# Kernel optimization log

Measured on AMD Instinct MI355X. Metric: run time of the kernel, lower is better.

## Reference

```python
import jax, jax.numpy as jnp
import numpy as np
from jax import lax

D = 1024
K = 3
LN_EPS = 1e-5


def setup_inputs() -> dict:
    key = jax.random.key(0)
    ks = jax.random.split(key, 8)
    B, T = 8, 4096
    x = jax.random.normal(ks[0], (B, T, D), dtype=jnp.float32)
    s = 1.0 / np.sqrt(D)
    in_proj_w = jax.random.uniform(ks[1], (D, 2 * D), jnp.float32, -s, s)
    in_proj_b = jax.random.uniform(ks[2], (2 * D,), jnp.float32, -s, s)
    conv_w = jax.random.uniform(ks[3], (D, 1, K), jnp.float32, -1.0 / np.sqrt(K), 1.0 / np.sqrt(K))
    conv_b = jax.random.uniform(ks[4], (D,), jnp.float32, -1.0 / np.sqrt(K), 1.0 / np.sqrt(K))
    logit_a = jnp.zeros((D,), jnp.float32)
    ssm_b = jnp.full((D,), 0.1, jnp.float32)
    ssm_c = jnp.ones((D,), jnp.float32)
    ssm_d = jnp.zeros((D,), jnp.float32)
    out_proj_w = jax.random.uniform(ks[5], (D, D), jnp.float32, -s, s)
    out_proj_b = jax.random.uniform(ks[6], (D,), jnp.float32, -s, s)
    ln_w = jnp.ones((D,), jnp.float32)
    ln_b = jnp.zeros((D,), jnp.float32)
    return {"x": x, "in_proj_w": in_proj_w, "in_proj_b": in_proj_b,
            "conv_w": conv_w, "conv_b": conv_b, "logit_a": logit_a,
            "ssm_b": ssm_b, "ssm_c": ssm_c, "ssm_d": ssm_d,
            "out_proj_w": out_proj_w, "out_proj_b": out_proj_b,
            "ln_w": ln_w, "ln_b": ln_b}


def _dwconv(v, conv_w, conv_b):
    # v: (B, T, D) -> depthwise conv1d, kernel K, 'same' padding
    vt = jnp.transpose(v, (0, 2, 1))  # (B, D, T)
    out = lax.conv_general_dilated(
        vt, conv_w, window_strides=(1,), padding=[(K // 2, K // 2)],
        dimension_numbers=("NCH", "OIH", "NCH"), feature_group_count=D)
    out = out + conv_b[None, :, None]
    return jnp.transpose(out, (0, 2, 1))  # (B, T, D)


def reference(x, in_proj_w, in_proj_b, conv_w, conv_b, logit_a,
              ssm_b, ssm_c, ssm_d, out_proj_w, out_proj_b, ln_w, ln_b):
    B, T, _ = x.shape
    residual = x
    uv = x @ in_proj_w + in_proj_b                      # (B, T, 2D)
    u, v = uv[..., :D], uv[..., D:]
    v = jax.nn.silu(v)
    v_local = _dwconv(v, conv_w, conv_b)                # (B, T, D)

    a = jax.nn.sigmoid(logit_a).astype(v_local.dtype)
    # diagonal LTI scan: h_t = a*h_{t-1} + b*u_t ; y_t = c*h_t + d*u_t
    def step(h, vt):
        h = a * h + ssm_b * vt
        return h, ssm_c * h + ssm_d * vt
    h0 = jnp.zeros((B, D), v_local.dtype)
    _, y_seq = lax.scan(step, h0, jnp.transpose(v_local, (1, 0, 2)))
    y_seq = jnp.transpose(y_seq, (1, 0, 2))             # (B, T, D)

    out = u * jax.nn.silu(y_seq)
    out = out @ out_proj_w + out_proj_b                 # dropout: eval mode (identity)
    h = out + residual
    mu = jnp.mean(h, axis=-1, keepdims=True)
    var = jnp.mean(jnp.square(h - mu), axis=-1, keepdims=True)
    return (h - mu) * lax.rsqrt(var + LN_EPS) * ln_w + ln_b
```

## Files before the change

### kernel.cpp

```cpp
#include <hip/hip_runtime.h>
#include <cstdint>
#include <cstddef>

#define D_DIM   1024
#define TWO_D   2048
#define B_DIM   8
#define T_DIM   4096
#define BT_DIM  (B_DIM*T_DIM)
#define LN_EPS  1e-5f
#define NCHUNK  128
#define CLEN    (T_DIM/NCHUNK)

typedef __attribute__((ext_vector_type(8))) short bf16x8;
typedef __attribute__((ext_vector_type(4))) float f32x4;

__device__ __forceinline__ float bf2f(unsigned short u){
  union { unsigned int i; float f; } c; c.i = ((unsigned int)u) << 16; return c.f;
}
__device__ __forceinline__ unsigned short f2bf(float f){
  union { float f; unsigned int i; } c; c.f = f;
  unsigned int x = c.i;
  return (unsigned short)((x + 0x7fffu + ((x >> 16) & 1u)) >> 16);
}
__device__ __forceinline__ float sigmoidf_(float x){ return 1.f/(1.f+__expf(-x)); }
__device__ __forceinline__ float siluf_(float x){ return x/(1.f+__expf(-x)); }


__global__ void cvt_f32_bf16(const float* __restrict__ in, unsigned short* __restrict__ out, int n){
  int i = (blockIdx.x*blockDim.x + threadIdx.x)*4;
  const int stride = gridDim.x*blockDim.x*4;
  for (; i + 3 < n; i += stride){
    float4 f = *(const float4*)(in + i);
    ushort4 o; o.x=f2bf(f.x); o.y=f2bf(f.y); o.z=f2bf(f.z); o.w=f2bf(f.w);
    *(ushort4*)(out + i) = o;
  }
}

__global__ __launch_bounds__(256) void cvt_transpose(
    const float* __restrict__ W, unsigned short* __restrict__ Wt,
    int rows, int cols)
{
  __shared__ float tile[32][33];
  const int tx = threadIdx.x & 31;
  const int ty = threadIdx.x >> 5;
  const int tpc = cols >> 5;
  const int bc = blockIdx.x % tpc;
  const int br = blockIdx.x / tpc;
  const int gc = bc*32 + tx;
  const int gr = br*32;
#pragma unroll
  for (int i = 0; i < 32; i += 8)
    tile[ty + i][tx] = W[(size_t)(gr + ty + i)*cols + gc];
  __syncthreads();
#pragma unroll
  for (int i = 0; i < 32; i += 8)
    Wt[(size_t)(bc*32 + ty + i)*rows + gr + tx] = f2bf(tile[tx][ty + i]);
}

template<int EPI>
__global__ __launch_bounds__(1024) void gemm256(
    const unsigned short* __restrict__ A,
    const unsigned short* __restrict__ Bt,
    const float* __restrict__ bias,
    const float* __restrict__ resid,
    unsigned short* __restrict__ outU,
    unsigned short* __restrict__ outV,
    const int K, const int nbn)
{
  __shared__ __align__(16) unsigned short sA[2][2][8192];
  __shared__ __align__(16) unsigned short sB[2][2][8192];

#define BARRIER()   __builtin_amdgcn_s_barrier()
#define FENCE()     __builtin_amdgcn_sched_barrier(0)
#define WAIT_VM2()  do { asm volatile("s_waitcnt vmcnt(2)"); FENCE(); } while(0)
#define WAIT_VM0()  do { asm volatile("s_waitcnt vmcnt(0)"); FENCE(); } while(0)

  const int tid  = threadIdx.x;
  const int lane = tid & 63;
  const int wv   = tid >> 6;
  const int wr   = wv >> 2;
  const int wc   = wv & 3;
  const int fr   = lane & 15;
  const int fq   = lane >> 4;

  const int nwg = gridDim.x;
  const int cpx = nwg >> 3;
  const int wg  = (blockIdx.x & 7) * cpx + (blockIdx.x >> 3);
  const int bm = wg / nbn, bn = wg % nbn;

  const unsigned short* Ag = A  + (size_t)bm * 256 * K;
  const unsigned short* Bg = Bt + (size_t)bn * 256 * K;

  const int r0  = tid >> 2;
  const int c0  = tid & 3;
  const int cs0 = c0 ^ ((r0 >> 1) & 3);
  const int ld0 = tid * 8;

#define STAGE(ARR, srcp, kofs)                                                           \
  __builtin_amdgcn_global_load_lds(                                                     \
      (const __attribute__((address_space(1))) void*)((srcp) + (size_t)r0*K + (kofs) + cs0*8), \
      (__attribute__((address_space(3))) void*)(&(ARR)[ld0]), 16, 0, 0)

  const int swz  = fq ^ ((fr >> 1) & 3);
  const int offA = (wr*64 + fr) * 32 + swz * 8;
  const int offB = (wc*64 + fr) * 32 + swz * 8;

  f32x4 acc[4][4];
#pragma unroll
  for (int i = 0; i < 4; ++i)
#pragma unroll
    for (int j = 0; j < 4; ++j) acc[i][j] = {0.f,0.f,0.f,0.f};

  bf16x8 afr[4], bfr[4];

#define PHASE(PAR, KH, STAGE_STMT, TAIL_WAIT)                              \
  do {                                                                     \
    _Pragma("unroll")                                                      \
    for (int m2 = 0; m2 < 4; ++m2)                                         \
      afr[m2] = *(const bf16x8*)(&sA[PAR][KH][offA + m2*512]);             \
    _Pragma("unroll")                                                      \
    for (int n2 = 0; n2 < 4; ++n2)                                         \
      bfr[n2] = *(const bf16x8*)(&sB[PAR][KH][offB + n2*512]);             \
    STAGE_STMT;                                                            \
    __builtin_amdgcn_s_setprio(1);                                         \
    _Pragma("unroll")                                                      \
    for (int m2 = 0; m2 < 4; ++m2)                                         \
      _Pragma("unroll")                                                    \
      for (int n2 = 0; n2 < 4; ++n2)                                       \
        acc[m2][n2] = __builtin_amdgcn_mfma_f32_16x16x32_bf16(             \
            afr[m2], bfr[n2], acc[m2][n2], 0, 0, 0);                       \
    __builtin_amdgcn_s_setprio(0);                                         \
    TAIL_WAIT;                                                             \
    BARRIER();                                                             \
  } while(0)

  const int npairs = K >> 7;

  STAGE(sA[0][0], Ag, 0);
  STAGE(sB[0][0], Bg, 0);
  STAGE(sA[0][1], Ag, 32);
  STAGE(sB[0][1], Bg, 32);
  WAIT_VM2();
  BARRIER();

  for (int i = 0; i < npairs - 1; ++i){
    const int kbO = ((i << 1) + 1) << 6;
    const int kbE = ((i << 1) + 2) << 6;
    PHASE(0, 0, { STAGE(sA[1][0], Ag, kbO);      STAGE(sB[1][0], Bg, kbO);      }, WAIT_VM2());
    PHASE(0, 1, { STAGE(sA[1][1], Ag, kbO + 32); STAGE(sB[1][1], Bg, kbO + 32); }, WAIT_VM2());
    PHASE(1, 0, { STAGE(sA[0][0], Ag, kbE);      STAGE(sB[0][0], Bg, kbE);      }, WAIT_VM2());
    PHASE(1, 1, { STAGE(sA[0][1], Ag, kbE + 32); STAGE(sB[0][1], Bg, kbE + 32); }, WAIT_VM2());
  }
  PHASE(0, 0, { STAGE(sA[1][0], Ag, K - 64); STAGE(sB[1][0], Bg, K - 64); }, WAIT_VM2());
  PHASE(0, 1, { STAGE(sA[1][1], Ag, K - 32); STAGE(sB[1][1], Bg, K - 32); }, WAIT_VM2());
  PHASE(1, 0, , WAIT_VM0());
  PHASE(1, 1, , );

  const int nb = bn*256 + wc*64;
  const int mb = bm*256 + wr*64;
  float bsv[4];
#pragma unroll
  for (int ni = 0; ni < 4; ++ni) bsv[ni] = bias[nb + ni*16 + fr];

  if (EPI == 0){
    const bool isV = (nb >= D_DIM);
    unsigned short* dst = isV ? (outV + (nb - D_DIM)) : (outU + nb);
#pragma unroll
    for (int mi = 0; mi < 4; ++mi){
#pragma unroll
      for (int j = 0; j < 4; ++j){
        const int m = mb + mi*16 + fq*4 + j;
        unsigned short* row = dst + (size_t)m*D_DIM + fr;
#pragma unroll
        for (int ni = 0; ni < 4; ++ni){
          float cv = acc[mi][ni][j] + bsv[ni];
          row[ni*16] = f2bf(isV ? siluf_(cv) : cv);
        }
      }
    }
  } else {
#pragma unroll
    for (int mi = 0; mi < 4; ++mi){
#pragma unroll
      for (int j = 0; j < 4; ++j){
        const int m = mb + mi*16 + fq*4 + j;
        const float* rrow = resid + (size_t)m*D_DIM + nb + fr;
        unsigned short* orow = outU + (size_t)m*D_DIM + nb + fr;
#pragma unroll
        for (int ni = 0; ni < 4; ++ni)
          orow[ni*16] = f2bf(acc[mi][ni][j] + bsv[ni] + rrow[ni*16]);
      }
    }
  }
#undef PHASE
#undef STAGE
#undef BARRIER
#undef FENCE
#undef WAIT_VM2
#undef WAIT_VM0
}

__global__ __launch_bounds__(256) void scan_a(
    const unsigned short* __restrict__ v,
    const float* __restrict__ conv_w, const float* __restrict__ conv_b,
    const float* __restrict__ logit_a, const float* __restrict__ ssm_b,
    float* __restrict__ hend)
{
  const int b = blockIdx.x / NCHUNK;
  const int c = blockIdx.x % NCHUNK;
  const int d0 = threadIdx.x * 4;
  const int t0 = c * CLEN;
  const unsigned short* vb = v + (size_t)b * T_DIM * D_DIM;

  float w0[4], w1[4], w2[4], av[4], bv[4], cb[4];
#pragma unroll
  for (int i=0;i<4;i++){
    w0[i] = conv_w[(d0+i)*3+0];
    w1[i] = conv_w[(d0+i)*3+1];
    w2[i] = conv_w[(d0+i)*3+2];
    cb[i] = conv_b[d0+i];
    av[i] = sigmoidf_(logit_a[d0+i]);
    bv[i] = ssm_b[d0+i];
  }
  float vm1[4], v0[4], h[4] = {0.f,0.f,0.f,0.f};
  if (t0 == 0){
#pragma unroll
    for (int i=0;i<4;i++) vm1[i]=0.f;
  } else {
    ushort4 u = *(const ushort4*)(vb + (size_t)(t0-1)*D_DIM + d0);
    vm1[0]=bf2f(u.x); vm1[1]=bf2f(u.y); vm1[2]=bf2f(u.z); vm1[3]=bf2f(u.w);
  }
  {
    ushort4 u = *(const ushort4*)(vb + (size_t)t0*D_DIM + d0);
    v0[0]=bf2f(u.x); v0[1]=bf2f(u.y); v0[2]=bf2f(u.z); v0[3]=bf2f(u.w);
  }
#pragma unroll 8
  for (int t = t0; t < t0 + CLEN; ++t){
    float vp1[4];
    if (t + 1 < T_DIM){
      ushort4 u = *(const ushort4*)(vb + (size_t)(t+1)*D_DIM + d0);
      vp1[0]=bf2f(u.x); vp1[1]=bf2f(u.y); vp1[2]=bf2f(u.z); vp1[3]=bf2f(u.w);
    } else { vp1[0]=vp1[1]=vp1[2]=vp1[3]=0.f; }
#pragma unroll
    for (int i=0;i<4;i++){
      float vl = w0[i]*vm1[i] + w1[i]*v0[i] + w2[i]*vp1[i] + cb[i];
      h[i] = av[i]*h[i] + bv[i]*vl;
      vm1[i]=v0[i]; v0[i]=vp1[i];
    }
  }
  float* he = hend + ((size_t)b*NCHUNK + c)*D_DIM + d0;
#pragma unroll
  for (int i=0;i<4;i++) he[i] = h[i];
}

__global__ void scan_fix(const float* __restrict__ hend, const float* __restrict__ logit_a,
                         float* __restrict__ hinit)
{
  int idx = blockIdx.x*blockDim.x + threadIdx.x;
  if (idx >= B_DIM*D_DIM) return;
  const int b = idx / D_DIM, d = idx % D_DIM;
  const float a  = sigmoidf_(logit_a[d]);
  const float aL = __powf(a, (float)CLEN);
  const float* hep = hend  + (size_t)b*NCHUNK*D_DIM + d;
  float*       hip = hinit + (size_t)b*NCHUNK*D_DIM + d;
  float h = 0.f;
  for (int cb = 0; cb < NCHUNK; cb += 8){
    float buf[8];
#pragma unroll
    for (int j = 0; j < 8; ++j)
      buf[j] = hep[(size_t)(cb + j)*D_DIM];
#pragma unroll
    for (int j = 0; j < 8; ++j){
      hip[(size_t)(cb + j)*D_DIM] = h;
      h = aL*h + buf[j];
    }
  }
}

__global__ __launch_bounds__(256) void scan_c(
    const unsigned short* __restrict__ v,
    const unsigned short* __restrict__ ubuf,
    const float* __restrict__ conv_w, const float* __restrict__ conv_b,
    const float* __restrict__ logit_a, const float* __restrict__ ssm_b,
    const float* __restrict__ ssm_c, const float* __restrict__ ssm_d,
    const float* __restrict__ hinit,
    unsigned short* __restrict__ gated)
{
  const int b = blockIdx.x / NCHUNK;
  const int c = blockIdx.x % NCHUNK;
  const int d0 = threadIdx.x * 4;
  const int t0 = c * CLEN;
  const unsigned short* vb = v    + (size_t)b * T_DIM * D_DIM;
  const unsigned short* ub = ubuf + (size_t)b * T_DIM * D_DIM;
  unsigned short* gb       = gated+ (size_t)b * T_DIM * D_DIM;

  float w0[4], w1[4], w2[4], av[4], bv[4], cb[4], scv[4], sdv[4], h[4];
#pragma unroll
  for (int i=0;i<4;i++){
    w0[i] = conv_w[(d0+i)*3+0];
    w1[i] = conv_w[(d0+i)*3+1];
    w2[i] = conv_w[(d0+i)*3+2];
    cb[i] = conv_b[d0+i];
    av[i] = sigmoidf_(logit_a[d0+i]);
    bv[i] = ssm_b[d0+i];
    scv[i] = ssm_c[d0+i];
    sdv[i] = ssm_d[d0+i];
    h[i] = hinit[((size_t)b*NCHUNK + c)*D_DIM + d0 + i];
  }
  float vm1[4], v0[4];
  if (t0 == 0){
#pragma unroll
    for (int i=0;i<4;i++) vm1[i]=0.f;
  } else {
    ushort4 u = *(const ushort4*)(vb + (size_t)(t0-1)*D_DIM + d0);
    vm1[0]=bf2f(u.x); vm1[1]=bf2f(u.y); vm1[2]=bf2f(u.z); vm1[3]=bf2f(u.w);
  }
  {
    ushort4 u = *(const ushort4*)(vb + (size_t)t0*D_DIM + d0);
    v0[0]=bf2f(u.x); v0[1]=bf2f(u.y); v0[2]=bf2f(u.z); v0[3]=bf2f(u.w);
  }
#pragma unroll 8
  for (int t = t0; t < t0 + CLEN; ++t){
    float vp1[4];
    if (t + 1 < T_DIM){
      ushort4 u = *(const ushort4*)(vb + (size_t)(t+1)*D_DIM + d0);
      vp1[0]=bf2f(u.x); vp1[1]=bf2f(u.y); vp1[2]=bf2f(u.z); vp1[3]=bf2f(u.w);
    } else { vp1[0]=vp1[1]=vp1[2]=vp1[3]=0.f; }
    ushort4 uu = *(const ushort4*)(ub + (size_t)t*D_DIM + d0);
    float uf[4] = { bf2f(uu.x), bf2f(uu.y), bf2f(uu.z), bf2f(uu.w) };
    ushort4 go;
    unsigned short gtmp[4];
#pragma unroll
    for (int i=0;i<4;i++){
      float vl = w0[i]*vm1[i] + w1[i]*v0[i] + w2[i]*vp1[i] + cb[i];
      h[i] = av[i]*h[i] + bv[i]*vl;
      float y = scv[i]*h[i] + sdv[i]*vl;
      gtmp[i] = f2bf(uf[i] * siluf_(y));
      vm1[i]=v0[i]; v0[i]=vp1[i];
    }
    go.x=gtmp[0]; go.y=gtmp[1]; go.z=gtmp[2]; go.w=gtmp[3];
    *(ushort4*)(gb + (size_t)t*D_DIM + d0) = go;
  }
}

__global__ __launch_bounds__(256) void ln_kernel(
    const unsigned short* __restrict__ hb, float* __restrict__ out,
    const float* __restrict__ lw, const float* __restrict__ lb)
{
  __shared__ float rs[4], rq[4];
  const int row = blockIdx.x;
  const int tid = threadIdx.x;
  const unsigned short* p = hb + (size_t)row * D_DIM;
  ushort4 u = *(const ushort4*)(p + tid*4);
  float x0 = bf2f(u.x), x1 = bf2f(u.y), x2 = bf2f(u.z), x3 = bf2f(u.w);
  float s = x0 + x1 + x2 + x3;
  float q = x0*x0 + x1*x1 + x2*x2 + x3*x3;
#pragma unroll
  for (int off = 32; off > 0; off >>= 1){
    s += __shfl_down(s, off, 64);
    q += __shfl_down(q, off, 64);
  }
  const int wv = tid >> 6;
  if ((tid & 63) == 0){ rs[wv] = s; rq[wv] = q; }
  __syncthreads();
  const float ts = rs[0]+rs[1]+rs[2]+rs[3];
  const float tq = rq[0]+rq[1]+rq[2]+rq[3];
  const float mu  = ts * (1.f/(float)D_DIM);
  const float var = tq * (1.f/(float)D_DIM) - mu*mu;
  const float inv = rsqrtf(var + LN_EPS);
  const float4 w4 = *(const float4*)(lw + tid*4);
  const float4 b4 = *(const float4*)(lb + tid*4);
  float4 o;
  o.x = (x0-mu)*inv*w4.x + b4.x;
  o.y = (x1-mu)*inv*w4.y + b4.y;
  o.z = (x2-mu)*inv*w4.z + b4.z;
  o.w = (x3-mu)*inv*w4.w + b4.w;
  *(float4*)(out + (size_t)row*D_DIM + tid*4) = o;
}

extern "C" void kernel_launch(void* const* d_in, const int* in_sizes, int n_in,
                              void* d_out, int out_size, void* d_ws, size_t ws_size,
                              hipStream_t stream)
{
  const float* x     = (const float*)d_in[0];
  const float* w1    = (const float*)d_in[1];
  const float* b1    = (const float*)d_in[2];
  const float* convw = (const float*)d_in[3];
  const float* convb = (const float*)d_in[4];
  const float* la    = (const float*)d_in[5];
  const float* sb    = (const float*)d_in[6];
  const float* sc    = (const float*)d_in[7];
  const float* sd    = (const float*)d_in[8];
  const float* w2    = (const float*)d_in[9];
  const float* b2    = (const float*)d_in[10];
  const float* lw    = (const float*)d_in[11];
  const float* lb    = (const float*)d_in[12];
  float* out = (float*)d_out;

  char* ws = (char*)d_ws;
  unsigned short* xb    = (unsigned short*)(ws + 0);
  unsigned short* ubf   = (unsigned short*)(ws + 67108864);
  unsigned short* vbf   = (unsigned short*)(ws + 134217728);
  unsigned short* w1t   = (unsigned short*)(ws + 201326592);
  unsigned short* w2t   = (unsigned short*)(ws + 205520896);
  float*          hend  = (float*)(ws + 207618048);
  float*          hinit = (float*)(ws + 211812352);

  cvt_f32_bf16<<<2048, 256, 0, stream>>>(x, xb, BT_DIM*D_DIM);
  cvt_transpose<<<(D_DIM/32)*(TWO_D/32), 256, 0, stream>>>(w1, w1t, D_DIM, TWO_D);
  cvt_transpose<<<(D_DIM/32)*(D_DIM/32), 256, 0, stream>>>(w2, w2t, D_DIM, D_DIM);

  gemm256<0><<<dim3((BT_DIM/256)*(TWO_D/256)), 1024, 0, stream>>>(
      xb, w1t, b1, nullptr, ubf, vbf, D_DIM, TWO_D/256);

  scan_a<<<B_DIM*NCHUNK, 256, 0, stream>>>(vbf, convw, convb, la, sb, hend);
  scan_fix<<<(B_DIM*D_DIM + 255)/256, 256, 0, stream>>>(hend, la, hinit);
  scan_c<<<B_DIM*NCHUNK, 256, 0, stream>>>(vbf, ubf, convw, convb, la, sb, sc, sd, hinit, xb);

  gemm256<1><<<dim3((BT_DIM/256)*(D_DIM/256)), 1024, 0, stream>>>(
      xb, w2t, b2, x, ubf, nullptr, D_DIM, D_DIM/256);

  ln_kernel<<<BT_DIM, 256, 0, stream>>>(ubf, out, lw, lb);
}
```

Measured before the change: 394.8 us.

## Halve GEMM barriers per K-tile and stagger half-tile order across odd/even waves

The GEMM main loop now issues one barrier per 64-wide K tile instead of one per 32-wide half. Odd waves read the two halves in the opposite order from even waves, which spreads LDS bank traffic and lets waves drift apart within a tile. The wait becomes vmcnt(0) before each barrier, so each prefetch has only one tile of compute to hide behind instead of overlapping across half-phases. This trades fewer synchronisations for shallower load/compute overlap.

```diff
diff --git a/kernel.cpp b/kernel.cpp
--- a/kernel.cpp
+++ b/kernel.cpp
@@ -72,8 +72,8 @@
 
 #define BARRIER()   __builtin_amdgcn_s_barrier()
 #define FENCE()     __builtin_amdgcn_sched_barrier(0)
+#define WAIT_VM0()  do { asm volatile("s_waitcnt vmcnt(0)"); FENCE(); } while(0)
 #define WAIT_VM2()  do { asm volatile("s_waitcnt vmcnt(2)"); FENCE(); } while(0)
-#define WAIT_VM0()  do { asm volatile("s_waitcnt vmcnt(0)"); FENCE(); } while(0)
 
   const int tid  = threadIdx.x;
   const int lane = tid & 63;
@@ -82,6 +82,7 @@
   const int wc   = wv & 3;
   const int fr   = lane & 15;
   const int fq   = lane >> 4;
+  const bool odd = (wv & 1) != 0;
 
   const int nwg = gridDim.x;
   const int cpx = nwg >> 3;
@@ -113,14 +114,14 @@
 
   bf16x8 afr[4], bfr[4];
 
-#define PHASE(PAR, KH, STAGE_STMT, TAIL_WAIT)                              \
+#define SUB(P, KH, STAGE_STMT)                                             \
   do {                                                                     \
     _Pragma("unroll")                                                      \
     for (int m2 = 0; m2 < 4; ++m2)                                         \
-      afr[m2] = *(const bf16x8*)(&sA[PAR][KH][offA + m2*512]);             \
+      afr[m2] = *(const bf16x8*)(&sA[P][KH][offA + m2*512]);               \
     _Pragma("unroll")                                                      \
     for (int n2 = 0; n2 < 4; ++n2)                                         \
-      bfr[n2] = *(const bf16x8*)(&sB[PAR][KH][offB + n2*512]);             \
+      bfr[n2] = *(const bf16x8*)(&sB[P][KH][offB + n2*512]);               \
     STAGE_STMT;                                                            \
     __builtin_amdgcn_s_setprio(1);                                         \
     _Pragma("unroll")                                                      \
@@ -130,8 +131,22 @@
         acc[m2][n2] = __builtin_amdgcn_mfma_f32_16x16x32_bf16(             \
             afr[m2], bfr[n2], acc[m2][n2], 0, 0, 0);                       \
     __builtin_amdgcn_s_setprio(0);                                         \
-    TAIL_WAIT;                                                             \
-    BARRIER();                                                             \
+  } while(0)
+
+#define TILE(P, NP, KB, LAST)                                              \
+  do {                                                                     \
+    if (!odd) {                                                            \
+      SUB(P, 0, if (!(LAST)) { STAGE(sA[NP][0], Ag, KB);                   \
+                               STAGE(sB[NP][0], Bg, KB); });               \
+      SUB(P, 1, if (!(LAST)) { STAGE(sA[NP][1], Ag, (KB) + 32);            \
+                               STAGE(sB[NP][1], Bg, (KB) + 32); });        \
+    } else {                                                               \
+      SUB(P, 1, if (!(LAST)) { STAGE(sA[NP][0], Ag, KB);                   \
+                               STAGE(sB[NP][0], Bg, KB); });               \
+      SUB(P, 0, if (!(LAST)) { STAGE(sA[NP][1], Ag, (KB) + 32);            \
+                               STAGE(sB[NP][1], Bg, (KB) + 32); });        \
+    }                                                                      \
+    if (!(LAST)) { WAIT_VM0(); BARRIER(); }                                \
   } while(0)
 
   const int npairs = K >> 7;
@@ -140,21 +155,17 @@
   STAGE(sB[0][0], Bg, 0);
   STAGE(sA[0][1], Ag, 32);
   STAGE(sB[0][1], Bg, 32);
-  WAIT_VM2();
+  WAIT_VM0();
   BARRIER();
 
   for (int i = 0; i < npairs - 1; ++i){
     const int kbO = ((i << 1) + 1) << 6;
     const int kbE = ((i << 1) + 2) << 6;
-    PHASE(0, 0, { STAGE(sA[1][0], Ag, kbO);      STAGE(sB[1][0], Bg, kbO);      }, WAIT_VM2());
-    PHASE(0, 1, { STAGE(sA[1][1], Ag, kbO + 32); STAGE(sB[1][1], Bg, kbO + 32); }, WAIT_VM2());
-    PHASE(1, 0, { STAGE(sA[0][0], Ag, kbE);      STAGE(sB[0][0], Bg, kbE);      }, WAIT_VM2());
-    PHASE(1, 1, { STAGE(sA[0][1], Ag, kbE + 32); STAGE(sB[0][1], Bg, kbE + 32); }, WAIT_VM2());
-  }
-  PHASE(0, 0, { STAGE(sA[1][0], Ag, K - 64); STAGE(sB[1][0], Bg, K - 64); }, WAIT_VM2());
-  PHASE(0, 1, { STAGE(sA[1][1], Ag, K - 32); STAGE(sB[1][1], Bg, K - 32); }, WAIT_VM2());
-  PHASE(1, 0, , WAIT_VM0());
-  PHASE(1, 1, , );
+    TILE(0, 1, kbO, 0);
+    TILE(1, 0, kbE, 0);
+  }
+  TILE(0, 1, K - 64, 0);
+  TILE(1, 0, 0, 1);
 
   const int nb = bn*256 + wc*64;
   const int mb = bm*256 + wr*64;
@@ -192,12 +203,13 @@
       }
     }
   }
-#undef PHASE
+#undef TILE
+#undef SUB
 #undef STAGE
 #undef BARRIER
 #undef FENCE
+#undef WAIT_VM0
 #undef WAIT_VM2
-#undef WAIT_VM0
 }
 
 __global__ __launch_bounds__(256) void scan_a(
```

After: 1.439 ms. 3.65x slower.
